# Optimization experiments

Hardware: AMD Instinct MI355X
Metric: run time of the kernel (lower is better)

The kernel has to match this reference:

```python
import jax, jax.numpy as jnp
import numpy as np

# Explicit-duration HSMM forward DP in log space.
# Recursion (all quantities in log space):
#   entry[t, j] = pi[j]                                   if t == 0
#               = logsumexp_i alpha[t-1, i] + A[i, j]      otherwise
#   alpha[t, j] = logsumexp_{d=1..min(Dmax, t+1)}
#                   entry[t-d+1, j] + D[j, d] + sum_{u=t-d+1..t} log_B[u, j]
#   loglik      = logsumexp_j alpha[T-1, j]

NEG = -1.0e30  # finite -inf sentinel (autodiff-safe)
B, T, S, DMAX = 64, 2048, 128, 128


def setup_inputs() -> dict:
    key = jax.random.key(0)
    k1, k2, k3, k4 = jax.random.split(key, 4)
    # emission log-likelihoods per (batch, time, state); need not normalize over states
    log_B = jax.random.normal(k1, (B, T, S), dtype=jnp.float32)
    # normalized log-prob buffers, matching the module's buffer constraints
    pi_logits = jax.nn.log_softmax(jax.random.normal(k2, (S,), dtype=jnp.float32))
    A_raw = jax.random.normal(k3, (S, S), dtype=jnp.float32)
    # SEMI transition constraint: no self-transitions (diagonal ~ -inf), rows normalized
    A_logits = jax.nn.log_softmax(
        jnp.where(jnp.eye(S, dtype=bool), -1.0e9, A_raw), axis=1)
    D_logits = jax.nn.log_softmax(
        jax.random.normal(k4, (S, DMAX), dtype=jnp.float32), axis=1)
    return {"log_B": log_B, "pi_logits": pi_logits,
            "A_logits": A_logits, "D_logits": D_logits}


def _hsmm_forward_loglik(log_B, pi_logits, A_logits, D_logits):
    Bn, Tn, Sn = log_B.shape
    Dm = D_logits.shape[1]
    lb = jnp.transpose(log_B, (1, 0, 2))                         # (T, B, S)
    # cum[k] = sum_{u < k} log_B[u]; front-padded with Dm zero rows (masked anyway)
    cum = jnp.concatenate(
        [jnp.zeros((1, Bn, Sn), lb.dtype), jnp.cumsum(lb, axis=0)], axis=0)
    cum_pad = jnp.concatenate(
        [jnp.zeros((Dm, Bn, Sn), lb.dtype), cum], axis=0)        # (T+Dm+1, B, S)
    logD = D_logits.T[:, None, :]                                # (Dm, 1, S)
    dur = jnp.arange(1, Dm + 1)[:, None, None]                   # (Dm, 1, 1)

    def step(carry, t):
        entry_buf, alpha_prev = carry                            # (Dm,B,S), (B,S)
        # transition into state j after a segment ended at t-1
        trans = jax.nn.logsumexp(
            alpha_prev[:, :, None] + A_logits[None, :, :], axis=1)  # (B, S)
        entry_t = jnp.where(t == 0, pi_logits[None, :], trans)
        # entry_buf[d-1] = entry[t-d+1]
        entry_buf = jnp.roll(entry_buf, 1, axis=0).at[0].set(entry_t)
        # segment emission sums: seg[d-1] = cum[t+1] - cum[t+1-d]
        win = jax.lax.dynamic_slice_in_dim(cum_pad, t + 1, Dm, axis=0)
        end = jax.lax.dynamic_slice_in_dim(cum_pad, t + Dm + 1, 1, axis=0)
        seg = end - jnp.flip(win, axis=0)                        # (Dm, B, S)
        scores = entry_buf + logD + seg
        scores = jnp.where(dur <= t + 1, scores, NEG)            # mask d > t+1
        alpha_t = jax.nn.logsumexp(scores, axis=0)               # (B, S)
        return (entry_buf, alpha_t), None

    init = (jnp.full((Dm, Bn, Sn), NEG, lb.dtype),
            jnp.full((Bn, Sn), NEG, lb.dtype))
    (_, alpha_last), _ = jax.lax.scan(step, init, jnp.arange(Tn))
    return jax.nn.logsumexp(alpha_last, axis=1)                  # (B,)


def reference(log_B, pi_logits, A_logits, D_logits):
    return _hsmm_forward_loglik(log_B, pi_logits, A_logits, D_logits)
```

## Files before the change

### kernel.cpp

```cpp
#include <hip/hip_runtime.h>

#define TT 2048
#define SS 128
#define DMAXX 128
#define NBATCH 64

typedef float f2 __attribute__((ext_vector_type(2)));

__device__ __forceinline__ float fexp2(float x){ return __builtin_amdgcn_exp2f(x); }
__device__ __forceinline__ float flog2(float x){ return __builtin_amdgcn_logf(x); }
__device__ __forceinline__ float frcp (float x){ return __builtin_amdgcn_rcpf(x); }

__device__ __forceinline__ f2 pk_mul(f2 a, f2 b){
    f2 d; asm("v_pk_mul_f32 %0, %1, %2" : "=v"(d) : "v"(a), "v"(b)); return d;
}
__device__ __forceinline__ f2 pk_fma(f2 a, f2 b, f2 c){
    f2 d; asm("v_pk_fma_f32 %0, %1, %2, %3" : "=v"(d) : "v"(a), "v"(b), "v"(c)); return d;
}

template<int CTRL>
__device__ __forceinline__ float dppf(float x) {
    int i = __float_as_int(x);
    return __int_as_float(__builtin_amdgcn_update_dpp(i, i, CTRL, 0xF, 0xF, false));
}
#define DPP_XOR1   0xB1
#define DPP_XOR2   0x4E
#define DPP_SHUP1  0x90
#define DPP_ROR4   0x124
#define DPP_ROR8   0x128
#define DPP_BC15   0x142
#define DPP_BC31   0x143

constexpr float LOG2E = 1.4426950408889634f;
constexpr float LN2   = 0.6931471805599453f;

struct State {
    f2    rp[16];
    f2    eAp[16];
    float eD[32];
    float eD0;
    float pf[4];
    float C2;
    float e_pi;
};

struct Ctx {
    const float4* up0; const float4* up1;
    const f2*     wmp;
    float* uaw0; float* uaw1;
    float* wmwp;
    bool q0, l63;
    const float* lb;
};

template<int PHI>
__device__ __forceinline__ void hsmm_step(State& st, const Ctx& c, int tb)
{
    constexpr int  rho   = 31 - PHI;
    constexpr int  pb    = (PHI + 1) & 1;
    constexpr int  wb    = PHI & 1;
    constexpr bool DO_WM = ((PHI & 7) == 6);
    constexpr bool DO_RN = ((PHI & 7) == 7);
    const int t = tb + PHI;

    const float4* up = pb ? c.up1 : c.up0;
    float4 v[8];
#pragma unroll
    for (int k = 0; k < 8; ++k) v[k] = up[k];

    float xB = st.pf[PHI & 3];
    if (t + 4 < TT) st.pf[PHI & 3] = c.lb[(size_t)(t + 4) * SS];
    float g = fexp2(xB * LOG2E);
    if constexpr (DO_RN) {
        f2 wv = *c.wmp;
        float m = fmaxf(wv.x, wv.y);
        m = fmaxf(m, dppf<DPP_XOR1>(m));
        m = fmaxf(m, dppf<DPP_XOR2>(m));
        st.C2 += flog2(m);
        g *= frcp(m);
    }

    float rold;
    if constexpr (rho & 1) rold = st.rp[rho >> 1].y; else rold = st.rp[rho >> 1].x;
    float car  = dppf<DPP_SHUP1>(rold);
    float insg = (c.q0 ? 0.f : car) * g;
    f2 gg; gg.x = g; gg.y = g;
#pragma unroll
    for (int m2 = 0; m2 < 16; ++m2) st.rp[m2] = pk_mul(st.rp[m2], gg);
    if constexpr (rho & 1) st.rp[rho >> 1].y = insg;
    else                   st.rp[rho >> 1].x = insg;

    float d0 = 0.f, d1 = 0.f, d2 = 0.f, d3 = 0.f;
#pragma unroll
    for (int m2 = 0; m2 < 16; m2 += 2) {
        d0 = fmaf(st.rp[m2].x,     st.eD[(2 * m2 + PHI + 1) & 31], d0);
        d1 = fmaf(st.rp[m2].y,     st.eD[(2 * m2 + PHI + 2) & 31], d1);
        d2 = fmaf(st.rp[m2 + 1].x, st.eD[(2 * m2 + PHI + 3) & 31], d2);
        d3 = fmaf(st.rp[m2 + 1].y, st.eD[(2 * m2 + PHI + 4) & 31], d3);
    }
    float ds = (d0 + d1) + (d2 + d3);
    ds += dppf<DPP_XOR1>(ds);
    ds += dppf<DPP_XOR2>(ds);

    f2 a0, a1, a2, a3;
    {
        f2 u;
        u.x = v[0].x; u.y = v[0].y; a0 = pk_mul(u, st.eAp[0]);
        u.x = v[0].z; u.y = v[0].w; a1 = pk_mul(u, st.eAp[1]);
        u.x = v[1].x; u.y = v[1].y; a2 = pk_mul(u, st.eAp[2]);
        u.x = v[1].z; u.y = v[1].w; a3 = pk_mul(u, st.eAp[3]);
#pragma unroll
        for (int kk = 2; kk < 8; kk += 2) {
            u.x = v[kk].x;     u.y = v[kk].y;     a0 = pk_fma(u, st.eAp[2 * kk],     a0);
            u.x = v[kk].z;     u.y = v[kk].w;     a1 = pk_fma(u, st.eAp[2 * kk + 1], a1);
            u.x = v[kk + 1].x; u.y = v[kk + 1].y; a2 = pk_fma(u, st.eAp[2 * kk + 2], a2);
            u.x = v[kk + 1].z; u.y = v[kk + 1].w; a3 = pk_fma(u, st.eAp[2 * kk + 3], a3);
        }
    }
    f2 asum = (a0 + a1) + (a2 + a3);
    float tp = asum.x + asum.y;
    tp += dppf<DPP_XOR1>(tp);
    tp += dppf<DPP_XOR2>(tp);
    if constexpr (PHI == 0) { if (tb == 0) tp = st.e_pi; }

    float tpg = tp * g;
    float U = fmaf(tpg, st.eD0, ds);
    if (c.q0) {
        if constexpr (rho & 1) st.rp[rho >> 1].y = tpg;
        else                   st.rp[rho >> 1].x = tpg;
    }
    if (c.q0) *(wb ? c.uaw1 : c.uaw0) = U;

    if constexpr (DO_WM) {
        float wm = U;
        wm = fmaxf(wm, dppf<DPP_ROR4>(wm));
        wm = fmaxf(wm, dppf<DPP_ROR8>(wm));
        wm = fmaxf(wm, dppf<DPP_BC15>(wm));
        wm = fmaxf(wm, dppf<DPP_BC31>(wm));
        if (c.l63) *c.wmwp = wm;
    }

    asm volatile("s_waitcnt lgkmcnt(0)\n\ts_barrier" ::: "memory");
}

__launch_bounds__(512, 2)
__global__ void hsmm_fwd_kernel(const float* __restrict__ logB,
                                const float* __restrict__ pi,
                                const float* __restrict__ A,
                                const float* __restrict__ D,
                                float* __restrict__ out)
{
    const int b   = blockIdx.x;
    const int tid = threadIdx.x;
    const int l   = tid & 63;
    const int w   = tid >> 6;
    const int j   = tid >> 2;
    const int q   = tid & 3;

    __shared__ __align__(16) float ua[2][4 * 36];
    __shared__ __align__(16) float wmaxf[8];

    State st;
#pragma unroll
    for (int k = 0; k < 16; ++k) {
        st.eAp[k].x = fexp2(A[(q * 32 + 2 * k)     * SS + j] * LOG2E);
        st.eAp[k].y = fexp2(A[(q * 32 + 2 * k + 1) * SS + j] * LOG2E);
    }
#pragma unroll
    for (int k = 0; k < 32; ++k)
        st.eD[k] = fexp2(D[j * DMAXX + q * 32 + k] * LOG2E);
#pragma unroll
    for (int k = 0; k < 16; ++k) { st.rp[k].x = 0.f; st.rp[k].y = 0.f; }
    st.eD0  = fexp2(D[j * DMAXX] * LOG2E);
    st.C2   = 0.f;
    st.e_pi = fexp2(pi[j] * LOG2E);

    const float* __restrict__ lb = logB + ((size_t)b * TT) * SS + j;
#pragma unroll
    for (int k = 0; k < 4; ++k) st.pf[k] = lb[(size_t)k * SS];

    Ctx c;
    c.up0  = (const float4*)&ua[0][q * 36];
    c.up1  = (const float4*)&ua[1][q * 36];
    c.wmp  = (const f2*)&wmaxf[2 * q];
    c.q0   = (q == 0);
    c.l63  = (l == 63);
    c.uaw0 = &ua[0][(j >> 5) * 36 + (j & 31)];
    c.uaw1 = &ua[1][(j >> 5) * 36 + (j & 31)];
    c.wmwp = &wmaxf[w];
    c.lb   = lb;


    for (int tb = 0; tb < TT; tb += 32) {
        hsmm_step< 0>(st, c, tb); hsmm_step< 1>(st, c, tb);
        hsmm_step< 2>(st, c, tb); hsmm_step< 3>(st, c, tb);
        hsmm_step< 4>(st, c, tb); hsmm_step< 5>(st, c, tb);
        hsmm_step< 6>(st, c, tb); hsmm_step< 7>(st, c, tb);
        hsmm_step< 8>(st, c, tb); hsmm_step< 9>(st, c, tb);
        hsmm_step<10>(st, c, tb); hsmm_step<11>(st, c, tb);
        hsmm_step<12>(st, c, tb); hsmm_step<13>(st, c, tb);
        hsmm_step<14>(st, c, tb); hsmm_step<15>(st, c, tb);
        hsmm_step<16>(st, c, tb); hsmm_step<17>(st, c, tb);
        hsmm_step<18>(st, c, tb); hsmm_step<19>(st, c, tb);
        hsmm_step<20>(st, c, tb); hsmm_step<21>(st, c, tb);
        hsmm_step<22>(st, c, tb); hsmm_step<23>(st, c, tb);
        hsmm_step<24>(st, c, tb); hsmm_step<25>(st, c, tb);
        hsmm_step<26>(st, c, tb); hsmm_step<27>(st, c, tb);
        hsmm_step<28>(st, c, tb); hsmm_step<29>(st, c, tb);
        hsmm_step<30>(st, c, tb); hsmm_step<31>(st, c, tb);
    }

    if (tid == 0) {
        float s = 0.f;
        for (int i = 0; i < SS; ++i) s += ua[1][(i >> 5) * 36 + (i & 31)];
        out[b] = (st.C2 + flog2(s)) * LN2;
    }
}

extern "C" void kernel_launch(void* const* d_in, const int* in_sizes, int n_in,
                              void* d_out, int out_size, void* d_ws, size_t ws_size,
                              hipStream_t stream) {
    const float* logB = (const float*)d_in[0];
    const float* pi   = (const float*)d_in[1];
    const float* A    = (const float*)d_in[2];
    const float* D    = (const float*)d_in[3];
    float* out        = (float*)d_out;
    hipLaunchKernelGGL(hsmm_fwd_kernel, dim3(NBATCH), dim3(512), 0, stream,
                       logB, pi, A, D, out);
}
```

Measured before the change: 1.028 ms.

## Restructure transition matvec to share LDS reads via DPP rotation across lanes

```diff
diff --git a/kernel.cpp b/kernel.cpp
--- a/kernel.cpp
+++ b/kernel.cpp
@@ -10,13 +10,7 @@
 __device__ __forceinline__ float fexp2(float x){ return __builtin_amdgcn_exp2f(x); }
 __device__ __forceinline__ float flog2(float x){ return __builtin_amdgcn_logf(x); }
 __device__ __forceinline__ float frcp (float x){ return __builtin_amdgcn_rcpf(x); }
-
-__device__ __forceinline__ f2 pk_mul(f2 a, f2 b){
-    f2 d; asm("v_pk_mul_f32 %0, %1, %2" : "=v"(d) : "v"(a), "v"(b)); return d;
-}
-__device__ __forceinline__ f2 pk_fma(f2 a, f2 b, f2 c){
-    f2 d; asm("v_pk_fma_f32 %0, %1, %2, %3" : "=v"(d) : "v"(a), "v"(b), "v"(c)); return d;
-}
+__device__ __forceinline__ f2 pkfma(f2 a, f2 b, f2 c){ return __builtin_elementwise_fma(a, b, c); }
 
 template<int CTRL>
 __device__ __forceinline__ float dppf(float x) {
@@ -36,21 +30,22 @@
 
 struct State {
     f2    rp[16];
-    f2    eAp[16];
+    f2    eAj[4][4];
     float eD[32];
     float eD0;
     float pf[4];
+    const float* pfp;
     float C2;
     float e_pi;
 };
 
 struct Ctx {
-    const float4* up0; const float4* up1;
+    const float4* upA0; const float4* upA1;
+    const float4* upB0; const float4* upB1;
     const f2*     wmp;
     float* uaw0; float* uaw1;
     float* wmwp;
     bool q0, l63;
-    const float* lb;
 };
 
 template<int PHI>
@@ -63,13 +58,12 @@
     constexpr bool DO_RN = ((PHI & 7) == 7);
     const int t = tb + PHI;
 
-    const float4* up = pb ? c.up1 : c.up0;
-    float4 v[8];
-#pragma unroll
-    for (int k = 0; k < 8; ++k) v[k] = up[k];
+    float4 vA = *(pb ? c.upA1 : c.upA0);
+    float4 vB = *(pb ? c.upB1 : c.upB0);
 
     float xB = st.pf[PHI & 3];
-    if (t + 4 < TT) st.pf[PHI & 3] = c.lb[(size_t)(t + 4) * SS];
+    if (t + 4 < TT) st.pf[PHI & 3] = st.pfp[0];
+    st.pfp += SS;
     float g = fexp2(xB * LOG2E);
     if constexpr (DO_RN) {
         f2 wv = *c.wmp;
@@ -84,9 +78,9 @@
     if constexpr (rho & 1) rold = st.rp[rho >> 1].y; else rold = st.rp[rho >> 1].x;
     float car  = dppf<DPP_SHUP1>(rold);
     float insg = (c.q0 ? 0.f : car) * g;
-    f2 gg; gg.x = g; gg.y = g;
-#pragma unroll
-    for (int m2 = 0; m2 < 16; ++m2) st.rp[m2] = pk_mul(st.rp[m2], gg);
+    f2 gg = {g, g};
+#pragma unroll
+    for (int m2 = 0; m2 < 16; ++m2) st.rp[m2] = st.rp[m2] * gg;
     if constexpr (rho & 1) st.rp[rho >> 1].y = insg;
     else                   st.rp[rho >> 1].x = insg;
 
@@ -102,23 +96,24 @@
     ds += dppf<DPP_XOR1>(ds);
     ds += dppf<DPP_XOR2>(ds);
 
-    f2 a0, a1, a2, a3;
-    {
-        f2 u;
-        u.x = v[0].x; u.y = v[0].y; a0 = pk_mul(u, st.eAp[0]);
-        u.x = v[0].z; u.y = v[0].w; a1 = pk_mul(u, st.eAp[1]);
-        u.x = v[1].x; u.y = v[1].y; a2 = pk_mul(u, st.eAp[2]);
-        u.x = v[1].z; u.y = v[1].w; a3 = pk_mul(u, st.eAp[3]);
-#pragma unroll
-        for (int kk = 2; kk < 8; kk += 2) {
-            u.x = v[kk].x;     u.y = v[kk].y;     a0 = pk_fma(u, st.eAp[2 * kk],     a0);
-            u.x = v[kk].z;     u.y = v[kk].w;     a1 = pk_fma(u, st.eAp[2 * kk + 1], a1);
-            u.x = v[kk + 1].x; u.y = v[kk + 1].y; a2 = pk_fma(u, st.eAp[2 * kk + 2], a2);
-            u.x = v[kk + 1].z; u.y = v[kk + 1].w; a3 = pk_fma(u, st.eAp[2 * kk + 3], a3);
-        }
-    }
-    f2 asum = (a0 + a1) + (a2 + a3);
-    float tp = asum.x + asum.y;
+    f2 r01 = {vA.x, vA.y}, r23 = {vA.z, vA.w};
+    f2 r45 = {vB.x, vB.y}, r67 = {vB.z, vB.w};
+    f2 acc =       r01 * st.eAj[0][0];
+    acc = pkfma(r23, st.eAj[0][1], acc);
+    acc = pkfma(r45, st.eAj[0][2], acc);
+    acc = pkfma(r67, st.eAj[0][3], acc);
+#pragma unroll
+    for (int h = 1; h < 4; ++h) {
+        acc.x = dppf<DPP_ROR4>(acc.x);
+        acc.y = dppf<DPP_ROR4>(acc.y);
+        acc = pkfma(r01, st.eAj[h][0], acc);
+        acc = pkfma(r23, st.eAj[h][1], acc);
+        acc = pkfma(r45, st.eAj[h][2], acc);
+        acc = pkfma(r67, st.eAj[h][3], acc);
+    }
+    acc.x = dppf<DPP_ROR4>(acc.x);
+    acc.y = dppf<DPP_ROR4>(acc.y);
+    float tp = acc.x + acc.y;
     tp += dppf<DPP_XOR1>(tp);
     tp += dppf<DPP_XOR2>(tp);
     if constexpr (PHI == 0) { if (tb == 0) tp = st.e_pi; }
@@ -157,20 +152,36 @@
     const int j   = tid >> 2;
     const int q   = tid & 3;
 
-    __shared__ __align__(16) float ua[2][4 * 36];
+    __shared__ __align__(16) float ua[2][SS];
     __shared__ __align__(16) float wmaxf[8];
 
+    int got4 = __builtin_amdgcn_update_dpp(l, l, DPP_ROR4, 0xF, 0xF, false);
+    bool dirA = (got4 == ((l & ~15) | ((l + 4) & 15)));
+
     State st;
-#pragma unroll
-    for (int k = 0; k < 16; ++k) {
-        st.eAp[k].x = fexp2(A[(q * 32 + 2 * k)     * SS + j] * LOG2E);
-        st.eAp[k].y = fexp2(A[(q * 32 + 2 * k + 1) * SS + j] * LOG2E);
+    {
+        const int m  = l & 15;
+        const int KA = l & 31;
+        const int KB = (l + 16) & 31;
+#pragma unroll
+        for (int h = 0; h < 4; ++h) {
+            int mv = dirA ? ((m + 4 * h) & 15) : ((m - 4 * h) & 15);
+            int u  = (l & ~15) | mv;
+            int jv = 16 * w + (u >> 2);
+#pragma unroll
+            for (int cc = 0; cc < 4; ++cc) {
+                int K  = (cc < 2) ? KA : KB;
+                int i0 = 4 * K + 2 * (cc & 1);
+                st.eAj[h][cc].x = fexp2(A[(i0)     * SS + jv] * LOG2E);
+                st.eAj[h][cc].y = fexp2(A[(i0 + 1) * SS + jv] * LOG2E);
+            }
+        }
     }
 #pragma unroll
     for (int k = 0; k < 32; ++k)
         st.eD[k] = fexp2(D[j * DMAXX + q * 32 + k] * LOG2E);
 #pragma unroll
-    for (int k = 0; k < 16; ++k) { st.rp[k].x = 0.f; st.rp[k].y = 0.f; }
+    for (int k = 0; k < 16; ++k) st.rp[k] = (f2){0.f, 0.f};
     st.eD0  = fexp2(D[j * DMAXX] * LOG2E);
     st.C2   = 0.f;
     st.e_pi = fexp2(pi[j] * LOG2E);
@@ -178,18 +189,19 @@
     const float* __restrict__ lb = logB + ((size_t)b * TT) * SS + j;
 #pragma unroll
     for (int k = 0; k < 4; ++k) st.pf[k] = lb[(size_t)k * SS];
+    st.pfp = lb + (size_t)4 * SS;
 
     Ctx c;
-    c.up0  = (const float4*)&ua[0][q * 36];
-    c.up1  = (const float4*)&ua[1][q * 36];
+    c.upA0 = (const float4*)&ua[0][4 * (l & 31)];
+    c.upA1 = (const float4*)&ua[1][4 * (l & 31)];
+    c.upB0 = (const float4*)&ua[0][4 * ((l + 16) & 31)];
+    c.upB1 = (const float4*)&ua[1][4 * ((l + 16) & 31)];
     c.wmp  = (const f2*)&wmaxf[2 * q];
     c.q0   = (q == 0);
     c.l63  = (l == 63);
-    c.uaw0 = &ua[0][(j >> 5) * 36 + (j & 31)];
-    c.uaw1 = &ua[1][(j >> 5) * 36 + (j & 31)];
+    c.uaw0 = &ua[0][j];
+    c.uaw1 = &ua[1][j];
     c.wmwp = &wmaxf[w];
-    c.lb   = lb;
-
 
     for (int tb = 0; tb < TT; tb += 32) {
         hsmm_step< 0>(st, c, tb); hsmm_step< 1>(st, c, tb);
@@ -212,7 +224,7 @@
 
     if (tid == 0) {
         float s = 0.f;
-        for (int i = 0; i < SS; ++i) s += ua[1][(i >> 5) * 36 + (i & 31)];
+        for (int i = 0; i < SS; ++i) s += ua[1][i];
         out[b] = (st.C2 + flog2(s)) * LN2;
     }
 }
```

Measured after the change: 1.104 ms. 1.07x slower.
